# Optimization experiments

Measured on AMD Instinct MI355X. Metric: run time of the kernel, lower is better.

Reference implementation:

```python
import jax, jax.numpy as jnp
import numpy as np
import math

B, L = 512, 50
NW, A, N, H = 50000, 512, 8, 256
EPS = 1e-5


def setup_inputs() -> dict:
    key = jax.random.key(0)
    ks = jax.random.split(key, 32)
    std = 1.0 / math.sqrt(H)
    nrm = lambda k, shape: jax.random.normal(k, shape, dtype=jnp.float32) * std
    inp = {}
    inp["inp_seq"] = jax.random.randint(ks[0], (B, L), 0, NW)
    inp["topic_mat"] = jax.random.normal(ks[1], (NW, A), dtype=jnp.float32)
    inp["dr_w"] = nrm(ks[2], (A, H))
    inp["dr_b"] = nrm(ks[3], (H,))
    inp["w1_w"] = nrm(ks[4], (N, H, H))
    inp["w1_b"] = nrm(ks[5], (N, H))
    inp["w2_w"] = nrm(ks[6], (N, H, H))
    inp["w2_b"] = nrm(ks[7], (N, H))
    inp["v_w"] = nrm(ks[8], (N, H))
    inp["lin0_w"] = nrm(ks[9], (2 * N * H, H))
    inp["lin0_b"] = nrm(ks[10], (H,))
    for i, base in zip((1, 2, 3), (11, 15, 19)):
        inp[f"l{i}_w"] = nrm(ks[base], (H, H))
        inp[f"l{i}_b"] = nrm(ks[base + 1], (H,))
        inp[f"g{i}"] = nrm(ks[base + 2], (H,))
        inp[f"be{i}"] = nrm(ks[base + 3], (H,))
    inp["out_w"] = nrm(ks[23], (H, NW - 1))
    return inp


def _bn(x, g, b):
    # BatchNorm1d, training mode: batch statistics (biased variance)
    m = jnp.mean(x, axis=0)
    v = jnp.var(x, axis=0)
    return (x - m) * jax.lax.rsqrt(v + EPS) * g + b


def reference(inp_seq, topic_mat, dr_w, dr_b, w1_w, w1_b, w2_w, w2_b, v_w,
              lin0_w, lin0_b, l1_w, l1_b, g1, be1, l2_w, l2_b, g2, be2,
              l3_w, l3_b, g3, be3, out_w):
    fea = jax.nn.relu(topic_mat[inp_seq] @ dr_w + dr_b)          # [B,L,H]
    mask = (inp_seq > 0).astype(fea.dtype)                        # [B,L]
    ht = fea[:, -1, :]                                            # [B,H]
    # all N heads batched: additive attention
    q1 = jnp.einsum('bh,nhd->bnd', ht, w1_w) + w1_b               # [B,N,H]
    q2 = jnp.einsum('blh,nhd->bnld', fea, w2_w) + w2_b[None, :, None, :]  # [B,N,L,H]
    alpha = jnp.einsum('bnlh,nh->bnl', jax.nn.sigmoid(q1[:, :, None, :] + q2), v_w)
    a = jnp.einsum('bnl,blh->bnh', alpha * mask[:, None, :], fea)  # [B,N,H]
    ht_rep = jnp.broadcast_to(ht[:, None, :], (a.shape[0], N, H))
    c_final = jnp.concatenate([a, ht_rep], axis=-1).reshape(a.shape[0], 2 * N * H)
    c = jax.nn.relu(c_final @ lin0_w + lin0_b)                    # [B,H]
    h = jax.nn.relu(_bn(c @ l1_w + l1_b, g1, be1))
    h = jax.nn.relu(_bn(h @ l2_w + l2_b, g2, be2))
    h = jax.nn.relu(_bn(h @ l3_w + l3_b, g3, be3))
    return (h + c) @ out_w                                        # [B, NW-1]
```

## Files before the change

kernel.cpp:

```cpp
#include <hip/hip_runtime.h>

typedef __attribute__((ext_vector_type(4))) float f32x4;
typedef __attribute__((ext_vector_type(4))) unsigned int u32x4;
typedef __attribute__((ext_vector_type(8))) short short8;
typedef __attribute__((ext_vector_type(4))) unsigned short u16x4;

#define DEV static __device__ __forceinline__

DEV unsigned short f2bf(float f) {
  union { float f; unsigned u; } v; v.f = f;
  unsigned r = v.u + 0x7fffu + ((v.u >> 16) & 1u);
  return (unsigned short)(r >> 16);
}
DEV float bf2f(unsigned short s) {
  union { unsigned u; float f; } v; v.u = ((unsigned)s) << 16;
  return v.f;
}

constexpr int KS = 32;
constexpr int LR = 40;

template<int BM, int BN, bool ABF16, bool GATHER, bool RELU, int OUTM, bool SPLITK = false>
__global__ __launch_bounds__(256)
void gemm_k(const void* __restrict__ Av, int lda, int rmul, int radd,
            const int* __restrict__ gidx,
            const float* __restrict__ Bp, int ldb,
            const float* __restrict__ bias,
            float* __restrict__ Cf, unsigned short* __restrict__ Cb, int ldc,
            int M, int N, int K)
{
  constexpr int WM = BM / 2, WN = BN / 2, FM = WM / 16, FN = WN / 16;
  __shared__ unsigned short As[2][BM][LR];
  __shared__ unsigned short Bs[2][BN][LR];
  const int tid = threadIdx.x;
  const int lane = tid & 63;
  const int wid = tid >> 6;
  const int wy = wid >> 1, wx = wid & 1;
  const long m0 = (long)blockIdx.x * BM;
  const int n0 = blockIdx.y * BN;
  const int kbeg = SPLITK ? blockIdx.z * K : 0;
  if constexpr (SPLITK) Cf += (long)blockIdx.z * M * ldc;

  f32x4 acc[FM][FN];
#pragma unroll
  for (int i = 0; i < FM; ++i)
#pragma unroll
    for (int j = 0; j < FN; ++j) acc[i][j] = (f32x4)0.f;

  const int nsteps = K / KS;

  auto stageA = [&](int ks, int buf) {
    const int k0 = kbeg + ks * KS;
    if constexpr (!ABF16) {
      const float* A = (const float*)Av;
#pragma unroll
      for (int p = 0; p < BM / 32; ++p) {
        const int r = p * 32 + (tid >> 3);
        const int kq = tid & 7;
        long ar = GATHER ? (long)gidx[m0 + r] : ((m0 + r) * (long)rmul + radd);
        f32x4 v = *(const f32x4*)(A + ar * lda + k0 + kq * 4);
        u16x4 o;
        o[0] = f2bf(v[0]); o[1] = f2bf(v[1]); o[2] = f2bf(v[2]); o[3] = f2bf(v[3]);
        *(u16x4*)(&As[buf][r][kq * 4]) = o;
      }
    } else {
      const unsigned short* A = (const unsigned short*)Av;
#pragma unroll
      for (int p = 0; p < BM / 64; ++p) {
        const int r = p * 64 + (tid >> 2);
        const int cq = tid & 3;
        long ar = (m0 + r) * (long)rmul + radd;
        u32x4 v = *(const u32x4*)(A + ar * lda + k0 + cq * 8);
        *(u32x4*)(&As[buf][r][cq * 8]) = v;
      }
    }
  };

  auto stageB = [&](int ks, int buf) {
    const int k0 = kbeg + ks * KS;
    constexpr int NC = BN / 4;
#pragma unroll
    for (int p = 0; p < (KS * NC) / 256; ++p) {
      const int n4 = tid % NC;
      const int k = p * (256 / NC) + tid / NC;
      const int c0 = n0 + n4 * 4;
      f32x4 v;
      if (c0 + 3 < N) {
        v = *(const f32x4*)(Bp + (long)(k0 + k) * ldb + c0);
      } else {
#pragma unroll
        for (int e = 0; e < 4; ++e)
          v[e] = (c0 + e < N) ? Bp[(long)(k0 + k) * ldb + c0 + e] : 0.f;
      }
      Bs[buf][n4 * 4 + 0][k] = f2bf(v[0]);
      Bs[buf][n4 * 4 + 1][k] = f2bf(v[1]);
      Bs[buf][n4 * 4 + 2][k] = f2bf(v[2]);
      Bs[buf][n4 * 4 + 3][k] = f2bf(v[3]);
    }
  };

  stageA(0, 0); stageB(0, 0);

  for (int ks = 0; ks < nsteps; ++ks) {
    __syncthreads();
    if (ks + 1 < nsteps) { stageA(ks + 1, (ks + 1) & 1); stageB(ks + 1, (ks + 1) & 1); }
    const int buf = ks & 1;
    short8 ar[FM], br[FN];
#pragma unroll
    for (int fm = 0; fm < FM; ++fm)
      ar[fm] = *(const short8*)(&As[buf][wy * WM + fm * 16 + (lane & 15)][(lane >> 4) * 8]);
#pragma unroll
    for (int fn = 0; fn < FN; ++fn)
      br[fn] = *(const short8*)(&Bs[buf][wx * WN + fn * 16 + (lane & 15)][(lane >> 4) * 8]);
#pragma unroll
    for (int fm = 0; fm < FM; ++fm)
#pragma unroll
      for (int fn = 0; fn < FN; ++fn)
        acc[fm][fn] = __builtin_amdgcn_mfma_f32_16x16x32_bf16(ar[fm], br[fn], acc[fm][fn], 0, 0, 0);
  }

#pragma unroll
  for (int fm = 0; fm < FM; ++fm) {
    const long row0 = m0 + wy * WM + fm * 16 + ((lane >> 4) << 2);
#pragma unroll
    for (int fn = 0; fn < FN; ++fn) {
      const int col = n0 + wx * WN + fn * 16 + (lane & 15);
      if (col >= N) continue;
      const float bv = bias ? bias[col] : 0.f;
#pragma unroll
      for (int j = 0; j < 4; ++j) {
        float v = acc[fm][fn][j] + bv;
        if constexpr (RELU) v = fmaxf(v, 0.f);
        const long r = row0 + j;
        if constexpr (OUTM & 1) Cf[r * ldc + col] = v;
        if constexpr (OUTM & 2) Cb[r * ldc + col] = f2bf(v);
      }
    }
  }
}

__global__ __launch_bounds__(256)
void alpha_k(const unsigned short* __restrict__ fea,
             const unsigned short* __restrict__ w2t,
             const float* __restrict__ q1buf,
             const float* __restrict__ vw,
             float* __restrict__ alpha)
{
  __shared__ unsigned short As[2][64][LR];
  __shared__ unsigned short Bs[2][256][LR];
  __shared__ float vws[256];
  __shared__ float red[4][64];
  const int tid = threadIdx.x;
  const int lane = tid & 63;
  const int w = tid >> 6;
  const int m0 = blockIdx.x * 64;
  const int n = blockIdx.y;

  vws[tid] = vw[n * 256 + tid];

  f32x4 acc[4][4];
#pragma unroll
  for (int i = 0; i < 4; ++i)
#pragma unroll
    for (int j = 0; j < 4; ++j) acc[i][j] = (f32x4)0.f;

  auto stageA = [&](int ks, int buf) {
    const int k0 = ks * KS;
    const int r = tid >> 2, cq = tid & 3;
    u32x4 v = *(const u32x4*)(fea + (long)(m0 + r) * 256 + k0 + cq * 8);
    *(u32x4*)(&As[buf][r][cq * 8]) = v;
  };
  auto stageB = [&](int ks, int buf) {
    const int k0 = ks * KS;
#pragma unroll
    for (int p = 0; p < 4; ++p) {
      const int r = p * 64 + (tid >> 2), cq = tid & 3;
      u32x4 v = *(const u32x4*)(w2t + ((long)(n * 256 + r)) * 256 + k0 + cq * 8);
      *(u32x4*)(&Bs[buf][r][cq * 8]) = v;
    }
  };

  stageA(0, 0); stageB(0, 0);
  for (int ks = 0; ks < 8; ++ks) {
    __syncthreads();
    if (ks < 7) { stageA(ks + 1, (ks + 1) & 1); stageB(ks + 1, (ks + 1) & 1); }
    const int buf = ks & 1;
    short8 ar[4], br[4];
#pragma unroll
    for (int fm = 0; fm < 4; ++fm)
      ar[fm] = *(const short8*)(&As[buf][fm * 16 + (lane & 15)][(lane >> 4) * 8]);
#pragma unroll
    for (int fn = 0; fn < 4; ++fn)
      br[fn] = *(const short8*)(&Bs[buf][w * 64 + fn * 16 + (lane & 15)][(lane >> 4) * 8]);
#pragma unroll
    for (int fm = 0; fm < 4; ++fm)
#pragma unroll
      for (int fn = 0; fn < 4; ++fn)
        acc[fm][fn] = __builtin_amdgcn_mfma_f32_16x16x32_bf16(ar[fm], br[fn], acc[fm][fn], 0, 0, 0);
  }

  const int g = lane >> 4, c = lane & 15;
  float part[4][4];
#pragma unroll
  for (int fm = 0; fm < 4; ++fm) {
#pragma unroll
    for (int j = 0; j < 4; ++j) {
      const int m = m0 + fm * 16 + g * 4 + j;
      const int b = m / 50;
      float p = 0.f;
#pragma unroll
      for (int fn = 0; fn < 4; ++fn) {
        const int col = w * 64 + fn * 16 + c;
        const float q = acc[fm][fn][j] + q1buf[(long)b * 2048 + n * 256 + col];
        const float s = 1.f / (1.f + __expf(-q));
        p += s * vws[col];
      }
      part[fm][j] = p;
    }
  }
#pragma unroll
  for (int fm = 0; fm < 4; ++fm)
#pragma unroll
    for (int j = 0; j < 4; ++j)
#pragma unroll
      for (int off = 1; off < 16; off <<= 1)
        part[fm][j] += __shfl_xor(part[fm][j], off);
  if (c == 0) {
#pragma unroll
    for (int fm = 0; fm < 4; ++fm)
#pragma unroll
      for (int j = 0; j < 4; ++j)
        red[w][fm * 16 + g * 4 + j] = part[fm][j];
  }
  __syncthreads();
  if (tid < 64) {
    const float s = red[0][tid] + red[1][tid] + red[2][tid] + red[3][tid];
    const int m = m0 + tid;
    const int b = m / 50, l = m - b * 50;
    alpha[((long)b * 8 + n) * 50 + l] = s;
  }
}

__global__ __launch_bounds__(256)
void cfinal_k(const unsigned short* __restrict__ fea,
              const float* __restrict__ alpha,
              const int* __restrict__ seq,
              unsigned short* __restrict__ cfin)
{
  __shared__ unsigned short feas[50][256];
  __shared__ float al[8][50];
  const int b = blockIdx.x, t = threadIdx.x;
#pragma unroll 1
  for (int l = 0; l < 50; ++l)
    feas[l][t] = fea[((long)b * 50 + l) * 256 + t];
  for (int i = t; i < 400; i += 256) {
    const int nn = i / 50, l = i - nn * 50;
    const float mk = (seq[b * 50 + l] > 0) ? 1.f : 0.f;
    al[nn][l] = alpha[((long)b * 8 + nn) * 50 + l] * mk;
  }
  __syncthreads();
#pragma unroll 1
  for (int nn = 0; nn < 8; ++nn) {
    float acc = 0.f;
#pragma unroll
    for (int l = 0; l < 50; ++l) acc += al[nn][l] * bf2f(feas[l][t]);
    cfin[(long)b * 2304 + nn * 256 + t] = f2bf(acc);
  }
  cfin[(long)b * 2304 + 2048 + t] = feas[49][t];
}

__global__ __launch_bounds__(256)
void lin0red_k(const float* __restrict__ part, const float* __restrict__ bias,
               float* __restrict__ cf, unsigned short* __restrict__ cb)
{
  const int e = blockIdx.x * 256 + threadIdx.x;
  float s = bias[e & 255];
#pragma unroll
  for (int z = 0; z < 8; ++z) s += part[z * 131072 + e];
  s = fmaxf(s, 0.f);
  cf[e] = s;
  cb[e] = f2bf(s);
}

template<bool LAST>
__global__ __launch_bounds__(256)
void bn_k(const float* __restrict__ y, const float* __restrict__ g,
          const float* __restrict__ be, const float* __restrict__ cres,
          unsigned short* __restrict__ out)
{
  const int t = threadIdx.x;
  const int col = blockIdx.x * 8 + (t & 7);
  const int rg = t >> 3;
  float v[16];
  float s = 0.f, q = 0.f;
#pragma unroll
  for (int i = 0; i < 16; ++i) {
    v[i] = y[(rg + i * 32) * 256 + col];
    s += v[i]; q += v[i] * v[i];
  }
  for (int off = 8; off < 64; off <<= 1) { s += __shfl_xor(s, off); q += __shfl_xor(q, off); }
  __shared__ float ps[4][8], pq[4][8], mm[8], rr[8];
  if ((t & 63) < 8) { ps[t >> 6][t & 7] = s; pq[t >> 6][t & 7] = q; }
  __syncthreads();
  if (t < 8) {
    const float S = ps[0][t] + ps[1][t] + ps[2][t] + ps[3][t];
    const float Q = pq[0][t] + pq[1][t] + pq[2][t] + pq[3][t];
    const float m = S * (1.f / 512.f);
    const float var = Q * (1.f / 512.f) - m * m;
    mm[t] = m;
    rr[t] = rsqrtf(var + 1e-5f);
  }
  __syncthreads();
  const float m = mm[t & 7], r = rr[t & 7], gg = g[col], bb = be[col];
#pragma unroll
  for (int i = 0; i < 16; ++i) {
    float h = (v[i] - m) * r * gg + bb;
    h = fmaxf(h, 0.f);
    if constexpr (LAST) h += cres[(rg + i * 32) * 256 + col];
    out[(rg + i * 32) * 256 + col] = f2bf(h);
  }
}

__global__ __launch_bounds__(256)
void prepack_k(const float* __restrict__ w1w, const float* __restrict__ w1b,
               const float* __restrict__ w2w, const float* __restrict__ w2b,
               float* __restrict__ w1t, float* __restrict__ bias12,
               unsigned short* __restrict__ w2t)
{
  const int tid = blockIdx.x * 256 + threadIdx.x;
  if (tid < 524288) {
    const int nn = tid >> 16, rem = tid & 65535, h = rem >> 8, d = rem & 255;
    w1t[h * 2048 + nn * 256 + d] = w1w[tid];
    w2t[((long)(nn * 256 + d)) * 256 + h] = f2bf(w2w[tid]);
  }
  if (tid < 2048) bias12[tid] = w1b[tid] + w2b[tid];
}

__global__ __launch_bounds__(256)
void prepack2_k(const float* __restrict__ lin0w, float* __restrict__ wcat)
{
  const int e = blockIdx.x * 256 + threadIdx.x;
  const int h2 = e >> 8, d = e & 255;
  float v;
  if (h2 < 2048) {
    const int n = h2 >> 8, h = h2 & 255;
    v = lin0w[((n * 512 + h) << 8) + d];
  } else {
    const int h = h2 - 2048;
    v = 0.f;
#pragma unroll
    for (int n = 0; n < 8; ++n) v += lin0w[((n * 512 + 256 + h) << 8) + d];
  }
  wcat[e] = v;
}

extern "C" void kernel_launch(void* const* d_in, const int* in_sizes, int n_in,
                              void* d_out, int out_size, void* d_ws, size_t ws_size,
                              hipStream_t stream)
{
  const int*   seq    = (const int*)  d_in[0];
  const float* topic  = (const float*)d_in[1];
  const float* dr_w   = (const float*)d_in[2];
  const float* dr_b   = (const float*)d_in[3];
  const float* w1_w   = (const float*)d_in[4];
  const float* w1_b   = (const float*)d_in[5];
  const float* w2_w   = (const float*)d_in[6];
  const float* w2_b   = (const float*)d_in[7];
  const float* v_w    = (const float*)d_in[8];
  const float* lin0_w = (const float*)d_in[9];
  const float* lin0_b = (const float*)d_in[10];
  const float* l1_w   = (const float*)d_in[11];
  const float* l1_b   = (const float*)d_in[12];
  const float* g1     = (const float*)d_in[13];
  const float* be1    = (const float*)d_in[14];
  const float* l2_w   = (const float*)d_in[15];
  const float* l2_b   = (const float*)d_in[16];
  const float* g2     = (const float*)d_in[17];
  const float* be2    = (const float*)d_in[18];
  const float* l3_w   = (const float*)d_in[19];
  const float* l3_b   = (const float*)d_in[20];
  const float* g3     = (const float*)d_in[21];
  const float* be3    = (const float*)d_in[22];
  const float* out_w  = (const float*)d_in[23];
  float* outp = (float*)d_out;

  char* ws = (char*)d_ws;
  size_t off = 0;
  auto alloc = [&](size_t bytes) -> void* {
    void* p = ws + off;
    off += (bytes + 255) & ~(size_t)255;
    return p;
  };
  unsigned short* fea    = (unsigned short*)alloc(25600ull * 256 * 2);
  unsigned short* w2t    = (unsigned short*)alloc(8ull * 256 * 256 * 2);
  float* w1t             = (float*)alloc(256ull * 2048 * 4);
  float* bias12          = (float*)alloc(2048ull * 4);
  float* q1buf           = (float*)alloc(512ull * 2048 * 4);
  float* alphab          = (float*)alloc(512ull * 8 * 50 * 4);
  unsigned short* cfin   = (unsigned short*)alloc(512ull * 2304 * 2);
  float* wcat            = (float*)alloc(2304ull * 256 * 4);
  float* part            = (float*)alloc(8ull * 512 * 256 * 4);
  float* c_f32           = (float*)alloc(512ull * 256 * 4);
  unsigned short* c_bf   = (unsigned short*)alloc(512ull * 256 * 2);
  unsigned short* h_bf   = (unsigned short*)alloc(512ull * 256 * 2);
  unsigned short* hc_bf  = (unsigned short*)alloc(512ull * 256 * 2);
  float* ybuf = part;

  hipLaunchKernelGGL(prepack_k, dim3(2048), dim3(256), 0, stream,
                     w1_w, w1_b, w2_w, w2_b, w1t, bias12, w2t);
  hipLaunchKernelGGL(prepack2_k, dim3(2304), dim3(256), 0, stream, lin0_w, wcat);

  hipLaunchKernelGGL((gemm_k<128,128,false,true,true,2>), dim3(200, 2), dim3(256), 0, stream,
                     (const void*)topic, 512, 1, 0, seq, dr_w, 256, dr_b,
                     (float*)nullptr, fea, 256, 25600, 256, 512);

  hipLaunchKernelGGL((gemm_k<64,64,true,false,false,1>), dim3(8, 32), dim3(256), 0, stream,
                     (const void*)fea, 256, 50, 49, (const int*)nullptr, w1t, 2048, bias12,
                     q1buf, (unsigned short*)nullptr, 2048, 512, 2048, 256);

  hipLaunchKernelGGL(alpha_k, dim3(400, 8), dim3(256), 0, stream,
                     fea, w2t, q1buf, v_w, alphab);

  hipLaunchKernelGGL(cfinal_k, dim3(512), dim3(256), 0, stream, fea, alphab, seq, cfin);

  hipLaunchKernelGGL((gemm_k<64,64,true,false,false,1,true>), dim3(8, 4, 8), dim3(256), 0, stream,
                     (const void*)cfin, 2304, 1, 0, (const int*)nullptr, wcat, 256,
                     (const float*)nullptr, part, (unsigned short*)nullptr, 256, 512, 256, 288);
  hipLaunchKernelGGL(lin0red_k, dim3(512), dim3(256), 0, stream, part, lin0_b, c_f32, c_bf);

  hipLaunchKernelGGL((gemm_k<64,64,true,false,false,1>), dim3(8, 4), dim3(256), 0, stream,
                     (const void*)c_bf, 256, 1, 0, (const int*)nullptr, l1_w, 256, l1_b,
                     ybuf, (unsigned short*)nullptr, 256, 512, 256, 256);
  hipLaunchKernelGGL((bn_k<false>), dim3(32), dim3(256), 0, stream,
                     ybuf, g1, be1, (const float*)nullptr, h_bf);

  hipLaunchKernelGGL((gemm_k<64,64,true,false,false,1>), dim3(8, 4), dim3(256), 0, stream,
                     (const void*)h_bf, 256, 1, 0, (const int*)nullptr, l2_w, 256, l2_b,
                     ybuf, (unsigned short*)nullptr, 256, 512, 256, 256);
  hipLaunchKernelGGL((bn_k<false>), dim3(32), dim3(256), 0, stream,
                     ybuf, g2, be2, (const float*)nullptr, h_bf);

  hipLaunchKernelGGL((gemm_k<64,64,true,false,false,1>), dim3(8, 4), dim3(256), 0, stream,
                     (const void*)h_bf, 256, 1, 0, (const int*)nullptr, l3_w, 256, l3_b,
                     ybuf, (unsigned short*)nullptr, 256, 512, 256, 256);
  hipLaunchKernelGGL((bn_k<true>), dim3(32), dim3(256), 0, stream,
                     ybuf, g3, be3, c_f32, hc_bf);

  hipLaunchKernelGGL((gemm_k<128,128,true,false,false,1>), dim3(4, 391), dim3(256), 0, stream,
                     (const void*)hc_bf, 256, 1, 0, (const int*)nullptr, out_w, 49999,
                     (const float*)nullptr, outp, (unsigned short*)nullptr, 49999, 512, 49999, 256);

  (void)in_sizes; (void)n_in; (void)out_size; (void)ws_size;
}
```

Before: 597.1 us.

## Prepack weights to bf16 tiles, split-K BN linears, swizzle output GEMM

Adds a packing kernel that converts dr_w and out_w to bf16 in a k-blocked layout so the GEMMs can stage B tiles with plain vector copies instead of per-element fp32-to-bf16 conversion and transposition. The gather GEMM uses a wider 64x256 tile and the big output GEMM remaps block ids across XCDs for cache locality. The three BN-preceded linears become split-K, with BN summing the partials and the linear biases omitted since batch-stat BN cancels them. This costs an extra pass over the large output weight each call.

Result: faster. 509.4 us (-14.7%).

```diff
diff --git a/kernel.cpp b/kernel.cpp
--- a/kernel.cpp
+++ b/kernel.cpp
@@ -20,24 +20,34 @@
 constexpr int KS = 32;
 constexpr int LR = 40;
 
-template<int BM, int BN, bool ABF16, bool GATHER, bool RELU, int OUTM, bool SPLITK = false>
-__global__ __launch_bounds__(256)
+template<int BM, int BN, int TH, int WY, int WX, bool ABF16, bool GATHER,
+         int BMODE, bool RELU, int OUTM, bool SPLITK, bool SWZ>
+__global__ __launch_bounds__(TH)
 void gemm_k(const void* __restrict__ Av, int lda, int rmul, int radd,
             const int* __restrict__ gidx,
-            const float* __restrict__ Bp, int ldb,
+            const void* __restrict__ Bp, int ldb,
             const float* __restrict__ bias,
             float* __restrict__ Cf, unsigned short* __restrict__ Cb, int ldc,
             int M, int N, int K)
 {
-  constexpr int WM = BM / 2, WN = BN / 2, FM = WM / 16, FN = WN / 16;
+  constexpr int WM = BM / WY, WN = BN / WX, FM = WM / 16, FN = WN / 16;
   __shared__ unsigned short As[2][BM][LR];
   __shared__ unsigned short Bs[2][BN][LR];
   const int tid = threadIdx.x;
   const int lane = tid & 63;
   const int wid = tid >> 6;
-  const int wy = wid >> 1, wx = wid & 1;
-  const long m0 = (long)blockIdx.x * BM;
-  const int n0 = blockIdx.y * BN;
+  const int wy = wid / WX, wx = wid % WX;
+  int bx = blockIdx.x, by = blockIdx.y;
+  if constexpr (SWZ) {
+    const int gx = gridDim.x, total = gx * gridDim.y;
+    const int bid = by * gx + bx;
+    const int q = total >> 3, r = total & 7;
+    const int xcd = bid & 7, idx = bid >> 3;
+    const int j = (xcd < r ? xcd * (q + 1) : r * (q + 1) + (xcd - r) * q) + idx;
+    bx = j % gx; by = j / gx;
+  }
+  const long m0 = (long)bx * BM;
+  const int n0 = by * BN;
   const int kbeg = SPLITK ? blockIdx.z * K : 0;
   if constexpr (SPLITK) Cf += (long)blockIdx.z * M * ldc;
 
@@ -54,8 +64,8 @@
     if constexpr (!ABF16) {
       const float* A = (const float*)Av;
 #pragma unroll
-      for (int p = 0; p < BM / 32; ++p) {
-        const int r = p * 32 + (tid >> 3);
+      for (int p = 0; p < BM / (TH / 8); ++p) {
+        const int r = p * (TH / 8) + (tid >> 3);
         const int kq = tid & 7;
         long ar = GATHER ? (long)gidx[m0 + r] : ((m0 + r) * (long)rmul + radd);
         f32x4 v = *(const f32x4*)(A + ar * lda + k0 + kq * 4);
@@ -66,8 +76,8 @@
     } else {
       const unsigned short* A = (const unsigned short*)Av;
 #pragma unroll
-      for (int p = 0; p < BM / 64; ++p) {
-        const int r = p * 64 + (tid >> 2);
+      for (int p = 0; p < BM / (TH / 4); ++p) {
+        const int r = p * (TH / 4) + (tid >> 2);
         const int cq = tid & 3;
         long ar = (m0 + r) * (long)rmul + radd;
         u32x4 v = *(const u32x4*)(A + ar * lda + k0 + cq * 8);
@@ -77,25 +87,38 @@
   };
 
   auto stageB = [&](int ks, int buf) {
-    const int k0 = kbeg + ks * KS;
-    constexpr int NC = BN / 4;
-#pragma unroll
-    for (int p = 0; p < (KS * NC) / 256; ++p) {
-      const int n4 = tid % NC;
-      const int k = p * (256 / NC) + tid / NC;
-      const int c0 = n0 + n4 * 4;
-      f32x4 v;
-      if (c0 + 3 < N) {
-        v = *(const f32x4*)(Bp + (long)(k0 + k) * ldb + c0);
-      } else {
-#pragma unroll
-        for (int e = 0; e < 4; ++e)
-          v[e] = (c0 + e < N) ? Bp[(long)(k0 + k) * ldb + c0 + e] : 0.f;
+    if constexpr (BMODE == 0) {
+      const float* B = (const float*)Bp;
+      const int k0 = kbeg + ks * KS;
+      constexpr int NC = BN / 4;
+#pragma unroll
+      for (int p = 0; p < (KS * NC) / TH; ++p) {
+        const int n4 = tid % NC;
+        const int k = p * (TH / NC) + tid / NC;
+        const int c0 = n0 + n4 * 4;
+        f32x4 v;
+        if (c0 + 3 < N) {
+          v = *(const f32x4*)(B + (long)(k0 + k) * ldb + c0);
+        } else {
+#pragma unroll
+          for (int e = 0; e < 4; ++e)
+            v[e] = (c0 + e < N) ? B[(long)(k0 + k) * ldb + c0 + e] : 0.f;
+        }
+        Bs[buf][n4 * 4 + 0][k] = f2bf(v[0]);
+        Bs[buf][n4 * 4 + 1][k] = f2bf(v[1]);
+        Bs[buf][n4 * 4 + 2][k] = f2bf(v[2]);
+        Bs[buf][n4 * 4 + 3][k] = f2bf(v[3]);
       }
-      Bs[buf][n4 * 4 + 0][k] = f2bf(v[0]);
-      Bs[buf][n4 * 4 + 1][k] = f2bf(v[1]);
-      Bs[buf][n4 * 4 + 2][k] = f2bf(v[2]);
-      Bs[buf][n4 * 4 + 3][k] = f2bf(v[3]);
+    } else {
+      const unsigned short* B = (const unsigned short*)Bp;
+      const int ksg = (kbeg / KS) + ks;
+#pragma unroll
+      for (int p = 0; p < (BN * 4) / TH; ++p) {
+        const int cc = p * (TH / 4) + (tid >> 2);
+        const int q = tid & 3;
+        u32x4 v = *(const u32x4*)(B + ((long)ksg * ldb + n0 + cc) * 32 + q * 8);
+        *(u32x4*)(&Bs[buf][cc][q * 8]) = v;
+      }
     }
   };
 
@@ -137,6 +160,21 @@
       }
     }
   }
+}
+
+__global__ __launch_bounds__(256)
+void packB_k(const float* __restrict__ src, unsigned short* __restrict__ dst,
+             int Nsrc, int Ndst)
+{
+  const int t = blockIdx.x * 256 + threadIdx.x;
+  const int ks = t / Ndst, n = t - ks * Ndst;
+  unsigned short buf[32];
+#pragma unroll
+  for (int kk = 0; kk < 32; ++kk)
+    buf[kk] = (n < Nsrc) ? f2bf(src[(long)(ks * 32 + kk) * Nsrc + n]) : (unsigned short)0;
+#pragma unroll
+  for (int q = 0; q < 4; ++q)
+    *(u32x4*)(dst + ((long)ks * Ndst + n) * 32 + q * 8) = *(const u32x4*)(buf + q * 8);
 }
 
 __global__ __launch_bounds__(256)
@@ -295,8 +333,10 @@
   float s = 0.f, q = 0.f;
 #pragma unroll
   for (int i = 0; i < 16; ++i) {
-    v[i] = y[(rg + i * 32) * 256 + col];
-    s += v[i]; q += v[i] * v[i];
+    const int off = (rg + i * 32) * 256 + col;
+    float x = y[off] + y[131072 + off] + y[262144 + off] + y[393216 + off];
+    v[i] = x;
+    s += x; q += x * x;
   }
   for (int off = 8; off < 64; off <<= 1) { s += __shfl_xor(s, off); q += __shfl_xor(q, off); }
   __shared__ float ps[4][8], pq[4][8], mm[8], rr[8];
@@ -370,15 +410,12 @@
   const float* lin0_w = (const float*)d_in[9];
   const float* lin0_b = (const float*)d_in[10];
   const float* l1_w   = (const float*)d_in[11];
-  const float* l1_b   = (const float*)d_in[12];
   const float* g1     = (const float*)d_in[13];
   const float* be1    = (const float*)d_in[14];
   const float* l2_w   = (const float*)d_in[15];
-  const float* l2_b   = (const float*)d_in[16];
   const float* g2     = (const float*)d_in[17];
   const float* be2    = (const float*)d_in[18];
   const float* l3_w   = (const float*)d_in[19];
-  const float* l3_b   = (const float*)d_in[20];
   const float* g3     = (const float*)d_in[21];
   const float* be3    = (const float*)d_in[22];
   const float* out_w  = (const float*)d_in[23];
@@ -404,18 +441,24 @@
   unsigned short* c_bf   = (unsigned short*)alloc(512ull * 256 * 2);
   unsigned short* h_bf   = (unsigned short*)alloc(512ull * 256 * 2);
   unsigned short* hc_bf  = (unsigned short*)alloc(512ull * 256 * 2);
-  float* ybuf = part;
+  unsigned short* drwp   = (unsigned short*)alloc(16ull * 256 * 32 * 2);
+  unsigned short* wpad   = (unsigned short*)alloc(8ull * 50048 * 32 * 2);
 
   hipLaunchKernelGGL(prepack_k, dim3(2048), dim3(256), 0, stream,
                      w1_w, w1_b, w2_w, w2_b, w1t, bias12, w2t);
   hipLaunchKernelGGL(prepack2_k, dim3(2304), dim3(256), 0, stream, lin0_w, wcat);
-
-  hipLaunchKernelGGL((gemm_k<128,128,false,true,true,2>), dim3(200, 2), dim3(256), 0, stream,
-                     (const void*)topic, 512, 1, 0, seq, dr_w, 256, dr_b,
+  hipLaunchKernelGGL(packB_k, dim3(16), dim3(256), 0, stream, dr_w, drwp, 256, 256);
+  hipLaunchKernelGGL(packB_k, dim3(1564), dim3(256), 0, stream, out_w, wpad, 49999, 50048);
+
+  hipLaunchKernelGGL((gemm_k<64,256,256,1,4, false,true, 1, true, 2, false,false>),
+                     dim3(400, 1), dim3(256), 0, stream,
+                     (const void*)topic, 512, 1, 0, seq, (const void*)drwp, 256, dr_b,
                      (float*)nullptr, fea, 256, 25600, 256, 512);
 
-  hipLaunchKernelGGL((gemm_k<64,64,true,false,false,1>), dim3(8, 32), dim3(256), 0, stream,
-                     (const void*)fea, 256, 50, 49, (const int*)nullptr, w1t, 2048, bias12,
+  hipLaunchKernelGGL((gemm_k<64,64,256,2,2, true,false, 0, false, 1, false,false>),
+                     dim3(8, 32), dim3(256), 0, stream,
+                     (const void*)fea, 256, 50, 49, (const int*)nullptr,
+                     (const void*)w1t, 2048, bias12,
                      q1buf, (unsigned short*)nullptr, 2048, 512, 2048, 256);
 
   hipLaunchKernelGGL(alpha_k, dim3(400, 8), dim3(256), 0, stream,
@@ -423,32 +466,42 @@
 
   hipLaunchKernelGGL(cfinal_k, dim3(512), dim3(256), 0, stream, fea, alphab, seq, cfin);
 
-  hipLaunchKernelGGL((gemm_k<64,64,true,false,false,1,true>), dim3(8, 4, 8), dim3(256), 0, stream,
-                     (const void*)cfin, 2304, 1, 0, (const int*)nullptr, wcat, 256,
-                     (const float*)nullptr, part, (unsigned short*)nullptr, 256, 512, 256, 288);
+  hipLaunchKernelGGL((gemm_k<64,64,256,2,2, true,false, 0, false, 1, true,false>),
+                     dim3(8, 4, 8), dim3(256), 0, stream,
+                     (const void*)cfin, 2304, 1, 0, (const int*)nullptr,
+                     (const void*)wcat, 256, (const float*)nullptr,
+                     part, (unsigned short*)nullptr, 256, 512, 256, 288);
   hipLaunchKernelGGL(lin0red_k, dim3(512), dim3(256), 0, stream, part, lin0_b, c_f32, c_bf);
 
-  hipLaunchKernelGGL((gemm_k<64,64,true,false,false,1>), dim3(8, 4), dim3(256), 0, stream,
-                     (const void*)c_bf, 256, 1, 0, (const int*)nullptr, l1_w, 256, l1_b,
-                     ybuf, (unsigned short*)nullptr, 256, 512, 256, 256);
+  hipLaunchKernelGGL((gemm_k<64,64,256,2,2, true,false, 0, false, 1, true,false>),
+                     dim3(8, 4, 4), dim3(256), 0, stream,
+                     (const void*)c_bf, 256, 1, 0, (const int*)nullptr,
+                     (const void*)l1_w, 256, (const float*)nullptr,
+                     part, (unsigned short*)nullptr, 256, 512, 256, 64);
   hipLaunchKernelGGL((bn_k<false>), dim3(32), dim3(256), 0, stream,
-                     ybuf, g1, be1, (const float*)nullptr, h_bf);
-
-  hipLaunchKernelGGL((gemm_k<64,64,true,false,false,1>), dim3(8, 4), dim3(256), 0, stream,
-                     (const void*)h_bf, 256, 1, 0, (const int*)nullptr, l2_w, 256, l2_b,
-                     ybuf, (unsigned short*)nullptr, 256, 512, 256, 256);
+                     part, g1, be1, (const float*)nullptr, h_bf);
+
+  hipLaunchKernelGGL((gemm_k<64,64,256,2,2, true,false, 0, false, 1, true,false>),
+                     dim3(8, 4, 4), dim3(256), 0, stream,
+                     (const void*)h_bf, 256, 1, 0, (const int*)nullptr,
+                     (const void*)l2_w, 256, (const float*)nullptr,
+                     part, (unsigned short*)nullptr, 256, 512, 256, 64);
   hipLaunchKernelGGL((bn_k<false>), dim3(32), dim3(256), 0, stream,
-                     ybuf, g2, be2, (const float*)nullptr, h_bf);
-
-  hipLaunchKernelGGL((gemm_k<64,64,true,false,false,1>), dim3(8, 4), dim3(256), 0, stream,
-                     (const void*)h_bf, 256, 1, 0, (const int*)nullptr, l3_w, 256, l3_b,
-                     ybuf, (unsigned short*)nullptr, 256, 512, 256, 256);
+                     part, g2, be2, (const float*)nullptr, h_bf);
+
+  hipLaunchKernelGGL((gemm_k<64,64,256,2,2, true,false, 0, false, 1, true,false>),
+                     dim3(8, 4, 4), dim3(256), 0, stream,
+                     (const void*)h_bf, 256, 1, 0, (const int*)nullptr,
+                     (const void*)l3_w, 256, (const float*)nullptr,
+                     part, (unsigned short*)nullptr, 256, 512, 256, 64);
   hipLaunchKernelGGL((bn_k<true>), dim3(32), dim3(256), 0, stream,
-                     ybuf, g3, be3, c_f32, hc_bf);
-
-  hipLaunchKernelGGL((gemm_k<128,128,true,false,false,1>), dim3(4, 391), dim3(256), 0, stream,
-                     (const void*)hc_bf, 256, 1, 0, (const int*)nullptr, out_w, 49999,
-                     (const float*)nullptr, outp, (unsigned short*)nullptr, 49999, 512, 49999, 256);
+                     part, g3, be3, c_f32, hc_bf);
+
+  hipLaunchKernelGGL((gemm_k<128,128,256,2,2, true,false, 1, false, 1, false,true>),
+                     dim3(4, 391), dim3(256), 0, stream,
+                     (const void*)hc_bf, 256, 1, 0, (const int*)nullptr,
+                     (const void*)wpad, 50048, (const float*)nullptr,
+                     outp, (unsigned short*)nullptr, 49999, 512, 49999, 256);
 
   (void)in_sizes; (void)n_in; (void)out_size; (void)ws_size;
 }
```
